# Kernel optimization log

Measured on AMD Instinct MI355X. Metric: run time of the kernel, lower is better.

Reference implementation:

```python
import jax, jax.numpy as jnp
import numpy as np

N, D = 262144, 64
NUM_CLASSES = 128
PROTOS_PER_CLASS = 4
P = NUM_CLASSES * PROTOS_PER_CLASS
ALPHA = 1.0


def setup_inputs() -> dict:
    key = jax.random.key(0)
    kx, kp, ky = jax.random.split(key, 3)
    x = jax.random.normal(kx, (N, D), dtype=jnp.float32)
    prototypes = jax.random.normal(kp, (P, D), dtype=jnp.float32)
    y = jax.random.randint(ky, (N,), 0, NUM_CLASSES, dtype=jnp.int32)
    return {"x": x, "prototypes": prototypes, "y": y}


def reference(x, prototypes, y):
    # prototype labels: i % num_classes (constant)
    proto_labels = jnp.arange(P, dtype=jnp.int32) % NUM_CLASSES  # [P]
    x_sq = jnp.sum(x * x, axis=1, keepdims=True)            # [N, 1]
    p_sq = jnp.sum(prototypes * prototypes, axis=1)          # [P]
    dist = x_sq + p_sq[None, :] - 2.0 * (x @ prototypes.T)   # [N, P]
    # masked dual-min over prototypes
    correct = proto_labels[None, :] == y[:, None]            # [N, P] bool
    inf = jnp.float32(jnp.inf)
    d1 = jnp.min(jnp.where(correct, dist, inf), axis=1)      # nearest same-class
    d2 = jnp.min(jnp.where(correct, inf, dist), axis=1)      # nearest other-class
    mu = (d1 - d2) / (d1 + d2 + 1e-9)
    return jnp.mean(jax.nn.sigmoid(ALPHA * mu))
```

## Files before the change

### kernel.cpp

```cpp
#include <hip/hip_runtime.h>
#include <math.h>

#define NROWS 262144
#define DDIM 64
#define NPROT 512
#define NBLK 1024

typedef __attribute__((ext_vector_type(8))) short short8;
typedef __attribute__((ext_vector_type(4))) float f32x4;

__device__ __forceinline__ unsigned short f2bf(float f) {
    union { float f; unsigned u; } c; c.f = f;
    unsigned r = c.u + 0x7FFFu + ((c.u >> 16) & 1u);
    return (unsigned short)(r >> 16);
}

__device__ __forceinline__ unsigned cvt_pk_bf16(float lo, float hi) {
    unsigned r;
    asm("v_cvt_pk_bf16_f32 %0, %1, %2" : "=v"(r) : "v"(lo), "v"(hi));
    return r;
}

template <int CTRL>
__device__ __forceinline__ float dpp_min(float v) {
    int s = __builtin_amdgcn_update_dpp(__float_as_int(v), __float_as_int(v),
                                        CTRL, 0xF, 0xF, true);
    return fminf(v, __int_as_float(s));
}

__global__ __launch_bounds__(64) void glvq_prep(
    const float* __restrict__ protos,
    float* __restrict__ psq_ws,
    uint4* __restrict__ pb_ws)
{
    const int p = blockIdx.x * 64 + threadIdx.x;
    const int jj = (p >> 4) & 7, col = p & 15, t = p >> 7;
    const int slot = jj * 64 + t * 16 + col;
    const float* pr = protos + p * DDIM;
    float sq = 0.f;
#pragma unroll
    for (int c = 0; c < 8; ++c) {
        float4 v0 = *reinterpret_cast<const float4*>(pr + c * 8);
        float4 v1 = *reinterpret_cast<const float4*>(pr + c * 8 + 4);
        sq += v0.x * v0.x + v0.y * v0.y + v0.z * v0.z + v0.w * v0.w +
              v1.x * v1.x + v1.y * v1.y + v1.z * v1.z + v1.w * v1.w;
        union { unsigned short s[8]; uint4 u; } pk;
        pk.s[0] = f2bf(-2.f * v0.x); pk.s[1] = f2bf(-2.f * v0.y);
        pk.s[2] = f2bf(-2.f * v0.z); pk.s[3] = f2bf(-2.f * v0.w);
        pk.s[4] = f2bf(-2.f * v1.x); pk.s[5] = f2bf(-2.f * v1.y);
        pk.s[6] = f2bf(-2.f * v1.z); pk.s[7] = f2bf(-2.f * v1.w);
        pb_ws[(slot * 8 + c) ^ (slot & 7)] = pk.u;
    }
    psq_ws[jj * 64 + col * 4 + t] = sq;
}

__global__ __launch_bounds__(256, 2) void glvq_main(
    const float* __restrict__ x,
    const int* __restrict__ y,
    const float* __restrict__ psq_ws,
    const uint4* __restrict__ pb_ws,
    float* __restrict__ partial)
{
    __shared__ uint4 s_pb[NPROT * 8];
    __shared__ float s_psq[NPROT];
    __shared__ float s_xsq[4][64];
    __shared__ int   s_y[256];
    __shared__ float s_red[4];

    const int tid = threadIdx.x;
    const int lane = tid & 63, w = tid >> 6;
    const int g = lane >> 4, col = lane & 15;
    const int row0 = blockIdx.x * 256;

    float4 raw[16];
    {
        const float* xb = x + (size_t)(row0 + w * 64 + col) * DDIM;
#pragma unroll
        for (int rt = 0; rt < 4; ++rt)
#pragma unroll
            for (int kk = 0; kk < 2; ++kk) {
                raw[rt * 4 + kk * 2 + 0] =
                    *reinterpret_cast<const float4*>(xb + rt * 1024 + kk * 32 + g * 8);
                raw[rt * 4 + kk * 2 + 1] =
                    *reinterpret_cast<const float4*>(xb + rt * 1024 + kk * 32 + g * 8 + 4);
            }
    }

#pragma unroll
    for (int i = 0; i < 16; ++i) s_pb[tid + 256 * i] = pb_ws[tid + 256 * i];
    s_psq[tid] = psq_ws[tid];
    s_psq[tid + 256] = psq_ws[tid + 256];
    s_y[tid] = y[row0 + tid];

    short8 afrag[4][2];
#pragma unroll
    for (int rt = 0; rt < 4; ++rt) {
        float part = 0.f;
#pragma unroll
        for (int kk = 0; kk < 2; ++kk) {
            float4 a0 = raw[rt * 4 + kk * 2 + 0];
            float4 a1 = raw[rt * 4 + kk * 2 + 1];
            part += a0.x * a0.x + a0.y * a0.y + a0.z * a0.z + a0.w * a0.w +
                    a1.x * a1.x + a1.y * a1.y + a1.z * a1.z + a1.w * a1.w;
            union { unsigned u[4]; short8 s; } pk;
            pk.u[0] = cvt_pk_bf16(a0.x, a0.y);
            pk.u[1] = cvt_pk_bf16(a0.z, a0.w);
            pk.u[2] = cvt_pk_bf16(a1.x, a1.y);
            pk.u[3] = cvt_pk_bf16(a1.z, a1.w);
            afrag[rt][kk] = pk.s;
        }
        part += __shfl_xor(part, 16);
        part += __shfl_xor(part, 32);
        if (g == 0) s_xsq[w][rt * 16 + col] = part;
    }

    __syncthreads();

    int jcv[4][4];
#pragma unroll
    for (int rt = 0; rt < 4; ++rt)
#pragma unroll
        for (int r = 0; r < 4; ++r) {
            int yv = s_y[w * 64 + rt * 16 + g * 4 + r];
            jcv[rt][r] = ((yv & 15) == col) ? (yv >> 4) : 15;
        }

    float m1[4][4], m2[4][4];
#pragma unroll
    for (int rt = 0; rt < 4; ++rt)
#pragma unroll
        for (int r = 0; r < 4; ++r) { m1[rt][r] = INFINITY; m2[rt][r] = INFINITY; }

    const int sw = (col & 7) << 4;
    const char* s_pb_c = (const char*)s_pb;
    const char* pb0 = s_pb_c + col * 128 + ((g * 16) ^ sw);
    const char* pb1 = s_pb_c + col * 128 + ((g * 16 + 64) ^ sw);
    const char* pqc = (const char*)s_psq + col * 16;

#pragma unroll
    for (int jj = 0; jj < 8; ++jj) {
        const int jjr = (jj + 2 * w) & 7;
        const int bj = jjr * 8192;
        const f32x4 psqv = *reinterpret_cast<const f32x4*>(pqc + jjr * 256);
        float vmin[4][4];
#pragma unroll
        for (int rt = 0; rt < 4; ++rt)
#pragma unroll
            for (int r = 0; r < 4; ++r) vmin[rt][r] = INFINITY;
#pragma unroll
        for (int t = 0; t < 4; ++t) {
            short8 b0 = *reinterpret_cast<const short8*>(pb0 + bj + t * 2048);
            short8 b1 = *reinterpret_cast<const short8*>(pb1 + bj + t * 2048);
            const float sd = psqv[t];
#pragma unroll
            for (int rt = 0; rt < 4; ++rt) {
                f32x4 a = {sd, sd, sd, sd};
                a = __builtin_amdgcn_mfma_f32_16x16x32_bf16(afrag[rt][0], b0, a, 0, 0, 0);
                a = __builtin_amdgcn_mfma_f32_16x16x32_bf16(afrag[rt][1], b1, a, 0, 0, 0);
#pragma unroll
                for (int r = 0; r < 4; ++r)
                    vmin[rt][r] = fminf(vmin[rt][r], a[r]);
            }
        }
#pragma unroll
        for (int rt = 0; rt < 4; ++rt)
#pragma unroll
            for (int r = 0; r < 4; ++r) {
                float v = vmin[rt][r];
                bool corr = (jcv[rt][r] == jjr);
                m1[rt][r] = corr ? v : m1[rt][r];
                m2[rt][r] = corr ? m2[rt][r] : fminf(m2[rt][r], v);
            }
    }

    float lsum = 0.f;
#pragma unroll
    for (int rt = 0; rt < 4; ++rt)
#pragma unroll
        for (int r = 0; r < 4; ++r) {
            float a1 = m1[rt][r], a2 = m2[rt][r];
            a1 = dpp_min<0xB1>(a1);  a2 = dpp_min<0xB1>(a2);
            a1 = dpp_min<0x4E>(a1);  a2 = dpp_min<0x4E>(a2);
            a1 = dpp_min<0x141>(a1); a2 = dpp_min<0x141>(a2);
            a1 = dpp_min<0x140>(a1); a2 = dpp_min<0x140>(a2);
            float xsq = s_xsq[w][rt * 16 + g * 4 + r];
            float d1 = xsq + a1, d2 = xsq + a2;
            float mu = (d1 - d2) / (d1 + d2 + 1e-9f);
            float sig = 1.f / (1.f + __expf(-mu));
            lsum += (col == 0) ? sig : 0.f;
        }
#pragma unroll
    for (int mk = 1; mk <= 32; mk <<= 1) lsum += __shfl_xor(lsum, mk);
    if (lane == 0) s_red[w] = lsum;
    __syncthreads();
    if (tid == 0)
        partial[blockIdx.x] = (s_red[0] + s_red[1]) + (s_red[2] + s_red[3]);
}

__global__ __launch_bounds__(256) void glvq_finalize(
    const float* __restrict__ partial, int nparts, float* __restrict__ out)
{
    __shared__ float s_red[256];
    const int tid = threadIdx.x;
    float acc = 0.f;
    for (int i = tid; i < nparts; i += 256) acc += partial[i];
    s_red[tid] = acc;
    __syncthreads();
#pragma unroll
    for (int s = 128; s >= 1; s >>= 1) {
        if (tid < s) s_red[tid] += s_red[tid + s];
        __syncthreads();
    }
    if (tid == 0) out[0] = s_red[0] * (1.0f / (float)NROWS);
}

extern "C" void kernel_launch(void* const* d_in, const int* in_sizes, int n_in,
                              void* d_out, int out_size, void* d_ws, size_t ws_size,
                              hipStream_t stream) {
    const float* x = (const float*)d_in[0];
    const float* protos = (const float*)d_in[1];
    const int* y = (const int*)d_in[2];
    float* out = (float*)d_out;

    float* partial = (float*)d_ws;
    float* psq_ws = partial + NBLK;
    uint4* pb_ws = (uint4*)((char*)d_ws + NBLK * 4 + NPROT * 4);

    glvq_prep<<<8, 64, 0, stream>>>(protos, psq_ws, pb_ws);
    glvq_main<<<NBLK, 256, 0, stream>>>(x, y, psq_ws, pb_ws, partial);
    glvq_finalize<<<1, 256, 0, stream>>>(partial, NBLK, out);
}
```

Before: 39.07 us.

## Process two row chunks per block, prefetching second chunk during first pass

Each block now handles 512 rows in two 256-row chunks. The second chunk's x rows are loaded into registers before the first chunk's MFMA pass runs, so the global load latency overlaps compute. The 64KB prototype tile is then staged into LDS once per 512 rows instead of once per 256 rows. The cost is higher register pressure from the extra 16 float4 buffers, and half as many blocks, which reduces parallelism on a GPU with many CUs.

After: 102.2 us. 2.62x slower.

```diff
diff --git a/kernel.cpp b/kernel.cpp
--- a/kernel.cpp
+++ b/kernel.cpp
@@ -4,7 +4,7 @@
 #define NROWS 262144
 #define DDIM 64
 #define NPROT 512
-#define NBLK 1024
+#define NBLK 512
 
 typedef __attribute__((ext_vector_type(8))) short short8;
 typedef __attribute__((ext_vector_type(4))) float f32x4;
@@ -54,45 +54,21 @@
     psq_ws[jj * 64 + col * 4 + t] = sq;
 }
 
-__global__ __launch_bounds__(256, 2) void glvq_main(
-    const float* __restrict__ x,
-    const int* __restrict__ y,
-    const float* __restrict__ psq_ws,
-    const uint4* __restrict__ pb_ws,
-    float* __restrict__ partial)
-{
-    __shared__ uint4 s_pb[NPROT * 8];
-    __shared__ float s_psq[NPROT];
-    __shared__ float s_xsq[4][64];
-    __shared__ int   s_y[256];
-    __shared__ float s_red[4];
-
-    const int tid = threadIdx.x;
-    const int lane = tid & 63, w = tid >> 6;
-    const int g = lane >> 4, col = lane & 15;
-    const int row0 = blockIdx.x * 256;
-
-    float4 raw[16];
-    {
-        const float* xb = x + (size_t)(row0 + w * 64 + col) * DDIM;
-#pragma unroll
-        for (int rt = 0; rt < 4; ++rt)
-#pragma unroll
-            for (int kk = 0; kk < 2; ++kk) {
-                raw[rt * 4 + kk * 2 + 0] =
-                    *reinterpret_cast<const float4*>(xb + rt * 1024 + kk * 32 + g * 8);
-                raw[rt * 4 + kk * 2 + 1] =
-                    *reinterpret_cast<const float4*>(xb + rt * 1024 + kk * 32 + g * 8 + 4);
-            }
-    }
-
-#pragma unroll
-    for (int i = 0; i < 16; ++i) s_pb[tid + 256 * i] = pb_ws[tid + 256 * i];
-    s_psq[tid] = psq_ws[tid];
-    s_psq[tid + 256] = psq_ws[tid + 256];
-    s_y[tid] = y[row0 + tid];
-
-    short8 afrag[4][2];
+__device__ __forceinline__ void load_x16(const float* xb, float4 (&raw)[16], int g) {
+#pragma unroll
+    for (int rt = 0; rt < 4; ++rt)
+#pragma unroll
+        for (int kk = 0; kk < 2; ++kk) {
+            raw[rt * 4 + kk * 2 + 0] =
+                *reinterpret_cast<const float4*>(xb + rt * 1024 + kk * 32 + g * 8);
+            raw[rt * 4 + kk * 2 + 1] =
+                *reinterpret_cast<const float4*>(xb + rt * 1024 + kk * 32 + g * 8 + 4);
+        }
+}
+
+__device__ __forceinline__ void convert_chunk(const float4 (&raw)[16],
+                                              short8 (&afrag)[4][2],
+                                              float* xsq_slot, int g, int col) {
 #pragma unroll
     for (int rt = 0; rt < 4; ++rt) {
         float part = 0.f;
@@ -111,31 +87,20 @@
         }
         part += __shfl_xor(part, 16);
         part += __shfl_xor(part, 32);
-        if (g == 0) s_xsq[w][rt * 16 + col] = part;
-    }
-
-    __syncthreads();
-
-    int jcv[4][4];
-#pragma unroll
-    for (int rt = 0; rt < 4; ++rt)
-#pragma unroll
-        for (int r = 0; r < 4; ++r) {
-            int yv = s_y[w * 64 + rt * 16 + g * 4 + r];
-            jcv[rt][r] = ((yv & 15) == col) ? (yv >> 4) : 15;
-        }
-
+        if (g == 0) xsq_slot[rt * 16 + col] = part;
+    }
+}
+
+__device__ __forceinline__ float chunk_pass(const short8 (&afrag)[4][2],
+                                            const int (&jcv)[4][4],
+                                            const char* pb0, const char* pb1,
+                                            const char* pqc, const float* xsq_row,
+                                            int w, int g, int col) {
     float m1[4][4], m2[4][4];
 #pragma unroll
     for (int rt = 0; rt < 4; ++rt)
 #pragma unroll
         for (int r = 0; r < 4; ++r) { m1[rt][r] = INFINITY; m2[rt][r] = INFINITY; }
-
-    const int sw = (col & 7) << 4;
-    const char* s_pb_c = (const char*)s_pb;
-    const char* pb0 = s_pb_c + col * 128 + ((g * 16) ^ sw);
-    const char* pb1 = s_pb_c + col * 128 + ((g * 16 + 64) ^ sw);
-    const char* pqc = (const char*)s_psq + col * 16;
 
 #pragma unroll
     for (int jj = 0; jj < 8; ++jj) {
@@ -183,12 +148,81 @@
             a1 = dpp_min<0x4E>(a1);  a2 = dpp_min<0x4E>(a2);
             a1 = dpp_min<0x141>(a1); a2 = dpp_min<0x141>(a2);
             a1 = dpp_min<0x140>(a1); a2 = dpp_min<0x140>(a2);
-            float xsq = s_xsq[w][rt * 16 + g * 4 + r];
+            float xsq = xsq_row[rt * 16 + g * 4 + r];
             float d1 = xsq + a1, d2 = xsq + a2;
             float mu = (d1 - d2) / (d1 + d2 + 1e-9f);
             float sig = 1.f / (1.f + __expf(-mu));
             lsum += (col == 0) ? sig : 0.f;
         }
+    return lsum;
+}
+
+__global__ __launch_bounds__(256, 2) void glvq_main(
+    const float* __restrict__ x,
+    const int* __restrict__ y,
+    const float* __restrict__ psq_ws,
+    const uint4* __restrict__ pb_ws,
+    float* __restrict__ partial)
+{
+    __shared__ uint4 s_pb[NPROT * 8];
+    __shared__ float s_psq[NPROT];
+    __shared__ float s_xsq[2][4][64];
+    __shared__ int   s_y[512];
+    __shared__ float s_red[4];
+
+    const int tid = threadIdx.x;
+    const int lane = tid & 63, w = tid >> 6;
+    const int g = lane >> 4, col = lane & 15;
+    const int row0 = blockIdx.x * 512;
+
+    const float* xb = x + (size_t)(row0 + w * 64 + col) * DDIM;
+
+    float4 raw[16];
+    load_x16(xb, raw, g);
+
+#pragma unroll
+    for (int i = 0; i < 16; ++i) s_pb[tid + 256 * i] = pb_ws[tid + 256 * i];
+    s_psq[tid] = psq_ws[tid];
+    s_psq[tid + 256] = psq_ws[tid + 256];
+    s_y[tid] = y[row0 + tid];
+    s_y[tid + 256] = y[row0 + 256 + tid];
+
+    short8 afrag[4][2];
+    convert_chunk(raw, afrag, &s_xsq[0][w][0], g, col);
+
+    __syncthreads();
+
+    int jcv[4][4];
+#pragma unroll
+    for (int rt = 0; rt < 4; ++rt)
+#pragma unroll
+        for (int r = 0; r < 4; ++r) {
+            int yv = s_y[w * 64 + rt * 16 + g * 4 + r];
+            jcv[rt][r] = ((yv & 15) == col) ? (yv >> 4) : 15;
+        }
+
+    float4 raw2[16];
+    load_x16(xb + 256 * DDIM, raw2, g);
+
+    const int sw = (col & 7) << 4;
+    const char* s_pb_c = (const char*)s_pb;
+    const char* pb0 = s_pb_c + col * 128 + ((g * 16) ^ sw);
+    const char* pb1 = s_pb_c + col * 128 + ((g * 16 + 64) ^ sw);
+    const char* pqc = (const char*)s_psq + col * 16;
+
+    float lsum = chunk_pass(afrag, jcv, pb0, pb1, pqc, &s_xsq[0][w][0], w, g, col);
+
+#pragma unroll
+    for (int rt = 0; rt < 4; ++rt)
+#pragma unroll
+        for (int r = 0; r < 4; ++r) {
+            int yv = s_y[256 + w * 64 + rt * 16 + g * 4 + r];
+            jcv[rt][r] = ((yv & 15) == col) ? (yv >> 4) : 15;
+        }
+    short8 afrag2[4][2];
+    convert_chunk(raw2, afrag2, &s_xsq[1][w][0], g, col);
+    lsum += chunk_pass(afrag2, jcv, pb0, pb1, pqc, &s_xsq[1][w][0], w, g, col);
+
 #pragma unroll
     for (int mk = 1; mk <= 32; mk <<= 1) lsum += __shfl_xor(lsum, mk);
     if (lane == 0) s_red[w] = lsum;
@@ -223,8 +257,8 @@
     float* out = (float*)d_out;
 
     float* partial = (float*)d_ws;
-    float* psq_ws = partial + NBLK;
-    uint4* pb_ws = (uint4*)((char*)d_ws + NBLK * 4 + NPROT * 4);
+    float* psq_ws = (float*)((char*)d_ws + 4096);
+    uint4* pb_ws = (uint4*)((char*)d_ws + 6144);
 
     glvq_prep<<<8, 64, 0, stream>>>(protos, psq_ws, pb_ws);
     glvq_main<<<NBLK, 256, 0, stream>>>(x, y, psq_ws, pb_ws, partial);
```
